# Kernel optimization log

Measured on AMD Instinct MI355X. Metric: run time of the kernel, lower is better.

The kernel has to match this reference:

```python
import jax, jax.numpy as jnp
import numpy as np
import math

N, CIN, COUT, K, H, W = 16, 512, 512, 1024, 64, 64


def setup_inputs() -> dict:
    key = jax.random.key(0)
    k0, k1, k2, k3, k4 = jax.random.split(key, 5)
    latent = jax.random.normal(k0, (N, CIN, H, W), dtype=jnp.float32)
    # kaiming_uniform_ on (K, COUT): bound = sqrt(6 / fan_in), fan_in = COUT
    cb_bound = math.sqrt(6.0 / COUT)
    codebook = jax.random.uniform(k1, (K, COUT), minval=-cb_bound, maxval=cb_bound, dtype=jnp.float32)
    # nn.Linear default init: uniform(-1/sqrt(fan_in), 1/sqrt(fan_in)), weight stored (out, in)
    wq = jax.random.uniform(k2, (COUT, CIN), minval=-1 / math.sqrt(CIN), maxval=1 / math.sqrt(CIN), dtype=jnp.float32)
    wk = jax.random.uniform(k3, (COUT, COUT), minval=-1 / math.sqrt(COUT), maxval=1 / math.sqrt(COUT), dtype=jnp.float32)
    wv = jax.random.uniform(k4, (COUT, COUT), minval=-1 / math.sqrt(COUT), maxval=1 / math.sqrt(COUT), dtype=jnp.float32)
    return {"latent": latent, "codebook": codebook, "wq": wq, "wk": wk, "wv": wv, "temperature": 1}


def _forward(latent, codebook, wq, wk, wv, temperature):
    n, cin, h, w = latent.shape
    kk, cout = codebook.shape
    scale = math.sqrt(cin)

    q = jnp.einsum("nchw,oc->nhwo", latent, wq)          # [n,h,w,cout]
    kmat = codebook @ wk.T                                   # [k,cout]
    v = codebook @ wv.T                                      # [k,cout]
    logit = jnp.einsum("nhwc,kc->nhwk", q, kmat) / scale  # [n,h,w,k]

    # ---- no-grad mask / histogram computation (dropout branch) ----
    lg = jax.lax.stop_gradient(logit)
    rk = jax.random.key(1234)
    r1, r2, r3 = jax.random.split(rk, 3)
    prob = jax.nn.softmax(lg, axis=-1)
    prob = jnp.where(prob < 1.0 / kk, 0.0, prob)
    mask = jax.random.bernoulli(r1, prob)                    # [n,h,w,k] bool
    trueCode = jnp.argmax(prob, axis=-1)                     # [n,h,w] int
    flat = trueCode.reshape(n, -1)
    binCount = jnp.zeros((n, kk), dtype=jnp.float32).at[jnp.arange(n)[:, None], flat].add(1.0)
    frequency = binCount[jnp.arange(n)[:, None, None], trueCode]  # [n,h,w]
    dropout = jax.random.bernoulli(r2, frequency / float(h * w))   # [n,h,w] bool
    scatterMask = jax.nn.one_hot(trueCode, kk, dtype=jnp.bool_) & dropout[..., None]
    mask = mask | scatterMask

    maskedLogit = jnp.where(mask, -1e9, logit)

    # ---- hard gumbel-softmax (straight-through) ----
    g = jax.random.gumbel(r3, maskedLogit.shape, dtype=maskedLogit.dtype)
    y_soft = jax.nn.softmax((maskedLogit + g) / temperature, axis=-1)
    y_hard = jax.nn.one_hot(jnp.argmax(y_soft, axis=-1), kk, dtype=y_soft.dtype)
    sample = y_hard - jax.lax.stop_gradient(y_soft) + y_soft

    result = jnp.einsum("nhwk,kc->nhwc", sample, v)
    quantized = jnp.transpose(result, (0, 3, 1, 2))          # [n,cout,h,w]
    code = jnp.argmax(sample, axis=-1)
    return quantized, code, logit, trueCode, frequency, binCount


def reference(latent, codebook, wq, wk, wv, temperature):
    return _forward(latent, codebook, wq, wk, wv, temperature)
```

## Files before the change

kernel.cpp:

```cpp
#include <hip/hip_runtime.h>
#include <stdint.h>
#include <stddef.h>

#define NB   16
#define CIN  512
#define COUT 512
#define KK   1024

#define MARGIN    2e-5f
#define INV_SCALE 0.04419417382415922f

typedef short short4v __attribute__((ext_vector_type(4)));
typedef short short8v __attribute__((ext_vector_type(8)));
typedef float f32x4  __attribute__((ext_vector_type(4)));

union Frag { short4v h[2]; short8v v8; };

__host__ __device__ inline void tf2x32(uint32_t k0, uint32_t k1,
                                       uint32_t x0, uint32_t x1,
                                       uint32_t& o0, uint32_t& o1) {
  uint32_t ks2 = k0 ^ k1 ^ 0x1BD11BDAu;
  x0 += k0; x1 += k1;
#define TF_RND(r) { x0 += x1; x1 = (x1 << r) | (x1 >> (32 - r)); x1 ^= x0; }
  TF_RND(13) TF_RND(15) TF_RND(26) TF_RND(6)
  x0 += k1;  x1 += ks2 + 1u;
  TF_RND(17) TF_RND(29) TF_RND(16) TF_RND(24)
  x0 += ks2; x1 += k0 + 2u;
  TF_RND(13) TF_RND(15) TF_RND(26) TF_RND(6)
  x0 += k0;  x1 += k1 + 3u;
  TF_RND(17) TF_RND(29) TF_RND(16) TF_RND(24)
  x0 += k1;  x1 += ks2 + 4u;
  TF_RND(13) TF_RND(15) TF_RND(26) TF_RND(6)
  x0 += ks2; x1 += k0 + 5u;
#undef TF_RND
  o0 = x0; o1 = x1;
}

__device__ inline float bits_to_u(uint32_t b) {
  return __uint_as_float((b >> 9) | 0x3f800000u) - 1.0f;
}

__device__ __host__ inline uint16_t f2bf(float f) {
  union { float f; uint32_t u; } c; c.f = f;
  uint32_t r = (c.u + 0x7fffu + ((c.u >> 16) & 1u)) >> 16;
  return (uint16_t)r;
}
__device__ inline float bf2f(uint16_t h) {
  union { uint32_t u; float f; } c; c.u = ((uint32_t)h) << 16;
  return c.f;
}

__device__ inline int permpos(int c) {
  const int base32 = c & ~31, within = c & 31;
  const int g = (within >> 2) & 3;
  const int e = (within & 16) ? (4 + (within & 3)) : (within & 3);
  return base32 + g * 8 + e;
}

__global__ __launch_bounds__(256) void k_combo(const float* __restrict__ cb,
                                               const float* __restrict__ wk,
                                               const float* __restrict__ wv,
                                               const float* __restrict__ latent,
                                               double* __restrict__ kmatT64,
                                               float* __restrict__ v,
                                               uint16_t* __restrict__ Apk) {
  __shared__ __align__(16) char sm[34816];
  const int t = threadIdx.x;
  if (blockIdx.x < 128) {
    float (*rows)[CIN] = (float(*)[CIN])sm;
    const int k0 = blockIdx.x * 8;
#pragma unroll
    for (int kk = 0; kk < 8; ++kk)
      for (int c = t; c < CIN; c += 256) rows[kk][c] = cb[(size_t)(k0 + kk) * CIN + c];
    __syncthreads();
#pragma unroll
    for (int oo = 0; oo < 2; ++oo) {
      const int o = t + oo * 256;
      const float* kr = wk + (size_t)o * CIN;
      const float* vr = wv + (size_t)o * CIN;
      double ak[8] = {0,0,0,0,0,0,0,0}, av[8] = {0,0,0,0,0,0,0,0};
      for (int c = 0; c < CIN; c += 4) {
        const float4 k4 = *(const float4*)(kr + c);
        const float4 v4 = *(const float4*)(vr + c);
#pragma unroll
        for (int kk = 0; kk < 8; ++kk) {
          const float4 c4 = *(const float4*)&rows[kk][c];
          ak[kk] += (double)c4.x * (double)k4.x + (double)c4.y * (double)k4.y
                  + (double)c4.z * (double)k4.z + (double)c4.w * (double)k4.w;
          av[kk] += (double)c4.x * (double)v4.x + (double)c4.y * (double)v4.y
                  + (double)c4.z * (double)v4.z + (double)c4.w * (double)v4.w;
        }
      }
#pragma unroll
      for (int kk = 0; kk < 8; ++kk) {
        kmatT64[(size_t)o * KK + k0 + kk] = ak[kk];
        v[(size_t)(k0 + kk) * COUT + o]  = (float)av[kk];
      }
    }
  } else {
    float (*T)[68] = (float(*)[68])sm;
    const int rb = blockIdx.x - 128, n = rb >> 6, h = rb & 63;
    for (int c0 = 0; c0 < 512; c0 += 128) {
      const int c2 = t >> 1, wh = (t & 1) * 32;
      const float* src = latent + (size_t)n * 2097152 + (size_t)(c0 + c2) * 4096 + h * 64 + wh;
#pragma unroll
      for (int i = 0; i < 8; ++i)
        *(float4*)&T[c2][wh + i*4] = *(const float4*)(src + i*4);
      __syncthreads();
      const int w = t & 63, cp = t >> 6;
      const int cs = (c0 >> 5) + cp;
      const int p = rb * 64 + w;
      uint16_t* dst = Apk + ((size_t)cs * 65536 + p) * 64;
#pragma unroll
      for (int q = 0; q < 8; ++q) {
        short8v vv;
#pragma unroll
        for (int j = 0; j < 4; ++j) {
          const float f = T[cp*32 + (q & 3) * 4 + (q >> 2) * 16 + j][w];
          const uint16_t hb = f2bf(f);
          vv[j]     = (short)hb;
          vv[4 + j] = (short)f2bf(f - bf2f(hb));
        }
        *(short8v*)(dst + q * 8) = vv;
      }
      __syncthreads();
    }
  }
}

__global__ __launch_bounds__(256) void k_wfold(const float* __restrict__ wq,
                                               const double* __restrict__ kmatT64,
                                               double* __restrict__ WT64,
                                               uint16_t* __restrict__ Wph,
                                               uint16_t* __restrict__ Wpl) {
  __shared__ __align__(16) float  As[16][64];
  __shared__ __align__(16) double Bs[16][128];
  const int t  = threadIdx.x;
  const int cb = (blockIdx.x >> 3) * 64;
  const int kb = (blockIdx.x & 7) * 128;
  const int tc = t >> 4, tk = t & 15;

  double acc[4][8];
#pragma unroll
  for (int i = 0; i < 4; ++i)
#pragma unroll
    for (int j = 0; j < 8; ++j) acc[i][j] = 0.0;

  for (int o0 = 0; o0 < COUT; o0 += 16) {
    {
      const int o2 = t >> 4, c4 = (t & 15) * 4;
      float4 f = *(const float4*)&wq[(size_t)(o0 + o2) * CIN + cb + c4];
      As[o2][c4+0] = f.x; As[o2][c4+1] = f.y; As[o2][c4+2] = f.z; As[o2][c4+3] = f.w;
    }
    {
      const int o2 = t >> 4, k8 = (t & 15) * 8;
      const double* src = &kmatT64[(size_t)(o0 + o2) * KK + kb + k8];
#pragma unroll
      for (int j = 0; j < 8; ++j) Bs[o2][k8 + j] = src[j];
    }
    __syncthreads();
#pragma unroll 4
    for (int o2 = 0; o2 < 16; ++o2) {
      double a[4], b[8];
#pragma unroll
      for (int i = 0; i < 4; ++i) a[i] = (double)As[o2][tc*4 + i];
#pragma unroll
      for (int j = 0; j < 8; ++j) b[j] = Bs[o2][tk*8 + j];
#pragma unroll
      for (int i = 0; i < 4; ++i)
#pragma unroll
        for (int j = 0; j < 8; ++j) acc[i][j] += a[i] * b[j];
    }
    __syncthreads();
  }
#pragma unroll
  for (int i = 0; i < 4; ++i) {
    const int c = cb + tc*4 + i;
    const int pp = permpos(c);
#pragma unroll
    for (int j = 0; j < 8; ++j) {
      const int k = kb + tk*8 + j;
      const double a = acc[i][j];
      WT64[(size_t)k * CIN + c] = a;
      const float wf = (float)a;
      const uint16_t hb = f2bf(wf);
      const float lof = wf - bf2f(hb);
      Wph[(size_t)k * CIN + pp] = hb;
      Wpl[(size_t)k * CIN + pp] = f2bf(lof);
    }
  }
}

#define STAGE_B(buf_, st_) do {                                            \
  const int kc_ = (st_) >> 4, cs_ = (st_) & 15;                            \
  _Pragma("unroll")                                                        \
  for (int i_ = 0; i_ < 8; ++i_) {                                         \
    const int half_ = i_ >> 2;                                             \
    const int D_ = (i_ & 3) * 4096 + wave * 1024 + lane * 16;              \
    const int kcol_ = D_ >> 6;                                             \
    const int bs_ = ((D_ >> 4) & 3) ^ ((kcol_ >> 1) & 3);                  \
    const uint16_t* gsrc_ = (half_ ? Wpl : Wph) +                          \
        ((size_t)(kc_ * 256 + kcol_) * 512 + cs_ * 32 + bs_ * 8);          \
    uint16_t* ldst_ = &Bst[buf_][half_ * 8192 + (D_ >> 1)];                \
    __builtin_amdgcn_global_load_lds(                                      \
        (const __attribute__((address_space(1))) uint32_t*)gsrc_,          \
        (__attribute__((address_space(3))) uint32_t*)ldst_, 16, 0, 0);     \
  } } while (0)

#define STAGE_A(buf_, st_) do {                                            \
  const int cs_ = (st_) & 15;                                              \
  _Pragma("unroll")                                                        \
  for (int i_ = 0; i_ < 2; ++i_) {                                         \
    const int D_ = i_ * 4096 + t * 16;                                     \
    const int row_ = D_ >> 7;                                              \
    const int q_ = ((D_ >> 4) & 7) ^ (row_ & 7);                           \
    const uint16_t* gsrc_ = Apk +                                          \
        ((size_t)cs_ * 65536 + pbase + row_) * 64 + q_ * 8;                \
    uint16_t* ldst_ = &Ast[buf_][D_ >> 1];                                 \
    __builtin_amdgcn_global_load_lds(                                      \
        (const __attribute__((address_space(1))) uint32_t*)gsrc_,          \
        (__attribute__((address_space(3))) uint32_t*)ldst_, 16, 0, 0);     \
  } } while (0)

__global__ __launch_bounds__(256, 2) void k_logit(
    const uint16_t* __restrict__ Apk,
    const uint16_t* __restrict__ Wph, const uint16_t* __restrict__ Wpl,
    const float* __restrict__ latent, const double* __restrict__ WT64,
    float* __restrict__ out_logit, int* __restrict__ trueCode, int* __restrict__ binCnt) {
  __shared__ __align__(16) char smem[81920];
  uint16_t (*Bst)[16384] = (uint16_t(*)[16384])smem;
  uint16_t (*Ast)[4096]  = (uint16_t(*)[4096])(smem + 65536);
  float* rv1     = (float*)(smem + 65536);
  int*   rk1     = (int*)  (smem + 65536 + 256);
  float* rv2     = (float*)(smem + 65536 + 512);
  int*   rk2     = (int*)  (smem + 65536 + 768);
  int*   candCnt = (int*)  (smem + 65536 + 1024);
  int  (*candK)[8] = (int(*)[8])(smem + 65536 + 1280);

  const int t = threadIdx.x;
  const int wave = t >> 6, lane = t & 63;
  const int wr = wave >> 1, wc = wave & 1;
  const int rb = blockIdx.x, n = rb >> 6;
  const int pbase = rb * 64;
  const int lg = lane >> 4, l15 = lane & 15;

  float v1_[2][4], v2_[2][4]; int k1_[2][4], k2_[2][4];
#pragma unroll
  for (int rt = 0; rt < 2; ++rt)
#pragma unroll
    for (int reg = 0; reg < 4; ++reg) {
      v1_[rt][reg] = -3.0e38f; k1_[rt][reg] = 0x7fffffff;
      v2_[rt][reg] = -3.0e38f; k2_[rt][reg] = 0x7fffffff;
    }

  f32x4 acc[2][8];

  STAGE_A(0, 0);
  STAGE_B(0, 0);
  __syncthreads();

  for (int st = 0; st < 64; ++st) {
    const int cur = st & 1, kc = st >> 4, cs = st & 15;
    if (cs == 0) {
#pragma unroll
      for (int rt = 0; rt < 2; ++rt)
#pragma unroll
        for (int ct = 0; ct < 8; ++ct) acc[rt][ct] = (f32x4){0.f, 0.f, 0.f, 0.f};
    }
    if (st < 63) { STAGE_A(cur ^ 1, st + 1); STAGE_B(cur ^ 1, st + 1); }

    Frag ah[2], al[2];
#pragma unroll
    for (int rt = 0; rt < 2; ++rt) {
      const int row = wr * 32 + rt * 16 + l15;
      const uint16_t* ab = &Ast[cur][row * 64];
      const int s0 = (lg ^ (row & 7)) * 8;
      Frag f0, f1;
      f0.v8 = *(const short8v*)(ab + s0);
      f1.v8 = *(const short8v*)(ab + (s0 ^ 32));
      ah[rt].h[0] = f0.h[0]; ah[rt].h[1] = f1.h[0];
      al[rt].h[0] = f0.h[1]; al[rt].h[1] = f1.h[1];
    }

#pragma unroll
    for (int ct = 0; ct < 8; ++ct) {
      const int kcol = wc * 128 + ct * 16 + l15;
      const int sw = lg ^ ((kcol >> 1) & 3);
      Frag bh, bl;
      bh.v8 = *(const short8v*)&Bst[cur][kcol * 32 + sw * 8];
      bl.v8 = *(const short8v*)&Bst[cur][8192 + kcol * 32 + sw * 8];
#pragma unroll
      for (int rt = 0; rt < 2; ++rt) {
        acc[rt][ct] = __builtin_amdgcn_mfma_f32_16x16x32_bf16(ah[rt].v8, bh.v8, acc[rt][ct], 0, 0, 0);
        acc[rt][ct] = __builtin_amdgcn_mfma_f32_16x16x32_bf16(ah[rt].v8, bl.v8, acc[rt][ct], 0, 0, 0);
        acc[rt][ct] = __builtin_amdgcn_mfma_f32_16x16x32_bf16(al[rt].v8, bh.v8, acc[rt][ct], 0, 0, 0);
      }
    }
    if (cs == 15) {
#pragma unroll
      for (int rt = 0; rt < 2; ++rt) {
#pragma unroll
        for (int reg = 0; reg < 4; ++reg) {
          const int prow = pbase + wr * 32 + rt * 16 + 4 * lg + reg;
          float* dst = out_logit + (size_t)prow * KK + kc * 256 + wc * 128 + l15;
          float v1 = v1_[rt][reg], v2 = v2_[rt][reg];
          int   k1 = k1_[rt][reg], k2 = k2_[rt][reg];
#pragma unroll
          for (int ct = 0; ct < 8; ++ct) {
            const float vv = acc[rt][ct][reg] * INV_SCALE;
            dst[ct * 16] = vv;
            const int kk = kc * 256 + wc * 128 + ct * 16 + l15;
            if (vv > v1 || (vv == v1 && kk < k1)) { v2 = v1; k2 = k1; v1 = vv; k1 = kk; }
            else if (vv > v2 || (vv == v2 && kk < k2)) { v2 = vv; k2 = kk; }
          }
          v1_[rt][reg] = v1; v2_[rt][reg] = v2;
          k1_[rt][reg] = k1; k2_[rt][reg] = k2;
        }
      }
    }
    __syncthreads();
  }

#pragma unroll
  for (int rt = 0; rt < 2; ++rt)
#pragma unroll
    for (int reg = 0; reg < 4; ++reg) {
      float v1 = v1_[rt][reg], v2 = v2_[rt][reg];
      int   k1 = k1_[rt][reg], k2 = k2_[rt][reg];
#pragma unroll
      for (int off = 1; off < 16; off <<= 1) {
        const float o1 = __shfl_xor(v1, off); const int ok1 = __shfl_xor(k1, off);
        const float o2 = __shfl_xor(v2, off); const int ok2 = __shfl_xor(k2, off);
        const bool aw = (v1 > o1) || (v1 == o1 && k1 < ok1);
        float n1, n2; int nk1, nk2;
        if (aw) {
          n1 = v1; nk1 = k1;
          if ((o1 > v2) || (o1 == v2 && ok1 < k2)) { n2 = o1; nk2 = ok1; }
          else { n2 = v2; nk2 = k2; }
        } else {
          n1 = o1; nk1 = ok1;
          if ((v1 > o2) || (v1 == o2 && k1 < ok2)) { n2 = v1; nk2 = k1; }
          else { n2 = o2; nk2 = ok2; }
        }
        v1 = n1; k1 = nk1; v2 = n2; k2 = nk2;
      }
      v1_[rt][reg] = v1; v2_[rt][reg] = v2;
      k1_[rt][reg] = k1; k2_[rt][reg] = k2;
    }
  if (wc == 0 && l15 == 0) {
#pragma unroll
    for (int rt = 0; rt < 2; ++rt)
#pragma unroll
      for (int reg = 0; reg < 4; ++reg) {
        const int r = wr * 32 + rt * 16 + 4 * lg + reg;
        rv1[r] = v1_[rt][reg]; rk1[r] = k1_[rt][reg];
        rv2[r] = v2_[rt][reg]; rk2[r] = k2_[rt][reg];
      }
  }
  __syncthreads();
  if (wc == 1 && l15 == 0) {
#pragma unroll
    for (int rt = 0; rt < 2; ++rt)
#pragma unroll
      for (int reg = 0; reg < 4; ++reg) {
        const int r = wr * 32 + rt * 16 + 4 * lg + reg;
        const float a1 = rv1[r], a2 = rv2[r];
        const int   ak1 = rk1[r], ak2 = rk2[r];
        const float b1 = v1_[rt][reg], b2 = v2_[rt][reg];
        const int   bk1 = k1_[rt][reg], bk2 = k2_[rt][reg];
        const bool aw = (a1 > b1) || (a1 == b1 && ak1 < bk1);
        float n1, n2; int nk1, nk2;
        if (aw) {
          n1 = a1; nk1 = ak1;
          if ((b1 > a2) || (b1 == a2 && bk1 < ak2)) { n2 = b1; nk2 = bk1; }
          else { n2 = a2; nk2 = ak2; }
        } else {
          n1 = b1; nk1 = bk1;
          if ((a1 > b2) || (a1 == b2 && ak1 < bk2)) { n2 = a1; nk2 = ak1; }
          else { n2 = b2; nk2 = bk2; }
        }
        rv1[r] = n1; rk1[r] = nk1; rv2[r] = n2; rk2[r] = nk2;
      }
  }
  __syncthreads();

  const int wv = t >> 6, lane_ = t & 63;
  for (int rr = 0; rr < 16; ++rr) {
    const int r = wv * 16 + rr;
    const int p = pbase + r;
    const float mv1 = rv1[r], mv2 = rv2[r];
    if (mv1 - mv2 > MARGIN) {
      if (lane_ == 0) {
        const int tc0 = rk1[r];
        trueCode[p] = tc0;
        atomicAdd(&binCnt[n * KK + tc0], 1);
      }
    } else {
      if (lane_ == 0) candCnt[r] = 0;
      __builtin_amdgcn_sched_barrier(0);
      asm volatile("s_waitcnt lgkmcnt(0)" ::: "memory");
      __builtin_amdgcn_sched_barrier(0);
      {
        const float thr = mv1 - MARGIN;
        const float* src = out_logit + (size_t)p * KK + lane_ * 16;
#pragma unroll
        for (int i = 0; i < 4; ++i) {
          const float4 f = *(const float4*)(src + i * 4);
          const int kb = lane_ * 16 + i * 4;
          if (f.x >= thr) { int id = atomicAdd(&candCnt[r], 1); if (id < 8) candK[r][id] = kb + 0; }
          if (f.y >= thr) { int id = atomicAdd(&candCnt[r], 1); if (id < 8) candK[r][id] = kb + 1; }
          if (f.z >= thr) { int id = atomicAdd(&candCnt[r], 1); if (id < 8) candK[r][id] = kb + 2; }
          if (f.w >= thr) { int id = atomicAdd(&candCnt[r], 1); if (id < 8) candK[r][id] = kb + 3; }
        }
      }
      __builtin_amdgcn_sched_barrier(0);
      asm volatile("s_waitcnt lgkmcnt(0)" ::: "memory");
      __builtin_amdgcn_sched_barrier(0);
      int cnt = candCnt[r]; if (cnt > 8) cnt = 8;
      const float* Ap = latent + (size_t)(p >> 12) * 2097152 + (p & 4095);
      int ks[8];
#pragma unroll
      for (int m = 0; m < 8; ++m) ks[m] = candK[r][m < cnt ? m : 0];
      double part[8] = {0, 0, 0, 0, 0, 0, 0, 0};
#pragma unroll
      for (int jj = 0; jj < 8; ++jj) {
        const int c = jj * 64 + lane_;
        const double lv = (double)Ap[(size_t)c * 4096];
#pragma unroll
        for (int m = 0; m < 8; ++m)
          if (m < cnt) part[m] += lv * WT64[(size_t)ks[m] * CIN + c];
      }
#pragma unroll
      for (int m = 0; m < 8; ++m)
        for (int off = 32; off; off >>= 1) part[m] += __shfl_xor(part[m], off);
      if (lane_ == 0) {
        double bv = -1.0e300; int bkk = KK;
#pragma unroll
        for (int m = 0; m < 8; ++m)
          if (m < cnt && (part[m] > bv || (part[m] == bv && ks[m] < bkk))) { bv = part[m]; bkk = ks[m]; }
        trueCode[p] = bkk;
        atomicAdd(&binCnt[n * KK + bkk], 1);
      }
    }
  }
}

__global__ __launch_bounds__(256) void k_final(const float* __restrict__ logit,
                                               const int* __restrict__ trueCode,
                                               const int* __restrict__ binCnt,
                                               float* __restrict__ out_code,
                                               float* __restrict__ out_tc,
                                               float* __restrict__ out_freq,
                                               int* __restrict__ code_int,
                                               uint32_t r1a, uint32_t r1b,
                                               uint32_t r2a, uint32_t r2b,
                                               uint32_t r3a, uint32_t r3b) {
  const int lane = threadIdx.x & 63;
  const int p = blockIdx.x * 4 + (threadIdx.x >> 6);
  const float* Lr = logit + (size_t)p * KK + lane * 16;

  float l[16];
#pragma unroll
  for (int i = 0; i < 4; ++i) {
    const float4 f = *(const float4*)(Lr + i * 4);
    l[i*4+0] = f.x; l[i*4+1] = f.y; l[i*4+2] = f.z; l[i*4+3] = f.w;
  }

  float m = l[0];
#pragma unroll
  for (int i = 1; i < 16; ++i) m = fmaxf(m, l[i]);
  for (int off = 32; off; off >>= 1) m = fmaxf(m, __shfl_xor(m, off));

  float e[16], s = 0.f;
#pragma unroll
  for (int i = 0; i < 16; ++i) { e[i] = __expf(l[i] - m); s += e[i]; }
  for (int off = 32; off; off >>= 1) s += __shfl_xor(s, off);

  const int tc = trueCode[p];
  const float fq = (float)binCnt[(p >> 12) * KK + tc];
  uint32_t d0, d1; tf2x32(r2a, r2b, 0u, (uint32_t)p, d0, d1);
  const bool drop = bits_to_u(d0 ^ d1) < fq * (1.0f / 4096.0f);

  const float thr = s * 0.0009765625f;
  float bv = -3.0e38f; int bk = 0;
#pragma unroll
  for (int j = 0; j < 16; ++j) {
    const int k = lane * 16 + j;
    const uint32_t idx = (uint32_t)(p * KK + k);
    uint32_t m0, m1, g0, g1;
    tf2x32(r1a, r1b, 0u, idx, m0, m1);
    tf2x32(r3a, r3b, 0u, idx, g0, g1);
    const bool mk = ((e[j] >= thr) && (bits_to_u(m0 ^ m1) * s < e[j])) || (k == tc && drop);
    const float u3  = fmaxf(bits_to_u(g0 ^ g1), 1.17549435082228751e-38f);
    const float gum = -__logf(-logf(u3));
    const float z = mk ? (gum - 1.0e9f) : (l[j] + gum);
    if (z > bv) { bv = z; bk = k; }
  }
  for (int off = 32; off; off >>= 1) {
    const float ov = __shfl_xor(bv, off);
    const int   ok = __shfl_xor(bk, off);
    if (ov > bv || (ov == bv && ok < bk)) { bv = ov; bk = ok; }
  }
  if (lane == 0) {
    out_code[p] = (float)bk; code_int[p] = bk;
    out_tc[p] = (float)tc;   out_freq[p] = fq;
  }
}

__global__ __launch_bounds__(256) void k_quant(const float* __restrict__ v,
                                               const int* __restrict__ code_int,
                                               float* __restrict__ outq) {
  __shared__ int codes[4096];
  const int n  = blockIdx.x >> 6;
  const int og = blockIdx.x & 63;
  const int t = threadIdx.x;
  const int4* cp = (const int4*)(code_int + (size_t)n * 4096);
#pragma unroll
  for (int i = 0; i < 4; ++i) ((int4*)codes)[t + i * 256] = cp[t + i * 256];
  __syncthreads();
  float* ob = outq + ((size_t)n * 512 + og * 8) * 4096;
  for (int c = 0; c < 4; ++c) {
    const int pos4 = (c * 256 + t) * 4;
    const int c0 = codes[pos4], c1 = codes[pos4 + 1], c2 = codes[pos4 + 2], c3 = codes[pos4 + 3];
    const float* v0 = v + (size_t)c0 * COUT;
    const float* v1 = v + (size_t)c1 * COUT;
    const float* v2 = v + (size_t)c2 * COUT;
    const float* v3 = v + (size_t)c3 * COUT;
#pragma unroll
    for (int oo = 0; oo < 8; ++oo) {
      const int o = og * 8 + oo;
      float4 val = make_float4(v0[o], v1[o], v2[o], v3[o]);
      *(float4*)(ob + (size_t)oo * 4096 + pos4) = val;
    }
  }
}

__global__ __launch_bounds__(256) void k_bincopy(const int* __restrict__ binCnt,
                                                 float* __restrict__ outb) {
  const int i = blockIdx.x * 256 + threadIdx.x;
  if (i < NB * KK) outb[i] = (float)binCnt[i];
}

extern "C" void kernel_launch(void* const* d_in, const int* in_sizes, int n_in,
                              void* d_out, int out_size, void* d_ws, size_t ws_size,
                              hipStream_t stream) {
  const float* latent   = (const float*)d_in[0];
  const float* codebook = (const float*)d_in[1];
  const float* wq       = (const float*)d_in[2];
  const float* wk       = (const float*)d_in[3];
  const float* wv       = (const float*)d_in[4];

  float* out = (float*)d_out;
  float* out_quant = out;
  float* out_code  = out + 33554432;
  float* out_logit = out + 33619968;
  float* out_tc    = out + 100728832;
  float* out_freq  = out + 100794368;
  float* out_bin   = out + 100859904;

  double*   WT64    = (double*)  out_quant;
  uint16_t* Wph     = (uint16_t*)(out_quant + 1048576);
  uint16_t* Wpl     = (uint16_t*)(out_quant + 1310720);
  double*   kmatT64 = (double*)  (out_quant + 1572864);

  char* ws = (char*)d_ws;
  uint16_t* Apk     = (uint16_t*)(ws);
  float*    v       = (float*)(ws + 134217728);
  int*      trueCode= (int*)  (ws + 136314880);
  int*      code_int= (int*)  (ws + 136577024);
  int*      binCnt  = (int*)  (ws + 136839168);

  uint32_t r1a, r1b, r2a, r2b, r3a, r3b;
  tf2x32(0u, 1234u, 0u, 0u, r1a, r1b);
  tf2x32(0u, 1234u, 0u, 1u, r2a, r2b);
  tf2x32(0u, 1234u, 0u, 2u, r3a, r3b);

  hipMemsetAsync(binCnt, 0, NB * KK * sizeof(int), stream);
  k_combo <<<1152,  256, 0, stream>>>(codebook, wk, wv, latent, kmatT64, v, Apk);
  k_wfold <<<64,    256, 0, stream>>>(wq, kmatT64, WT64, Wph, Wpl);
  k_logit <<<1024,  256, 0, stream>>>(Apk, Wph, Wpl, latent, WT64,
                                      out_logit, trueCode, binCnt);
  k_final <<<16384, 256, 0, stream>>>(out_logit, trueCode, binCnt,
                                      out_code, out_tc, out_freq, code_int,
                                      r1a, r1b, r2a, r2b, r3a, r3b);
  k_quant <<<1024,  256, 0, stream>>>(v, code_int, out_quant);
  k_bincopy<<<64,   256, 0, stream>>>(binCnt, out_bin);
}
```

Baseline: 909.2 us.

## Fuse gumbel sampling into logit kernel via two-candidate argmax, defer dropout pick

Moves the softmax/mask/gumbel argmax from the separate k_final kernel into the tail of k_logit. Because the dropout decision depends on global bin counts that are not known until k_logit finishes, each row keeps a top-two candidate: the code without dropout and the code if the true code were masked. A tiny k_pick kernel then chooses between them after the histogram is complete. The logit rows are re-read right after being written, so they are likely still in cache, and a full kernel launch over the logits is removed. The cost is extra register pressure and more work in the tail of k_logit, plus slightly more complex tie-breaking logic.

```diff
diff --git a/kernel.cpp b/kernel.cpp
--- a/kernel.cpp
+++ b/kernel.cpp
@@ -226,7 +226,9 @@
     const uint16_t* __restrict__ Apk,
     const uint16_t* __restrict__ Wph, const uint16_t* __restrict__ Wpl,
     const float* __restrict__ latent, const double* __restrict__ WT64,
-    float* __restrict__ out_logit, int* __restrict__ trueCode, int* __restrict__ binCnt) {
+    float* __restrict__ out_logit, int* __restrict__ trueCode, int* __restrict__ binCnt,
+    int* __restrict__ candA, int* __restrict__ candB,
+    uint32_t r1a, uint32_t r1b, uint32_t r3a, uint32_t r3b) {
   __shared__ __align__(16) char smem[81920];
   uint16_t (*Bst)[16384] = (uint16_t(*)[16384])smem;
   uint16_t (*Ast)[4096]  = (uint16_t(*)[4096])(smem + 65536);
@@ -440,71 +442,93 @@
           if (m < cnt && (part[m] > bv || (part[m] == bv && ks[m] < bkk))) { bv = part[m]; bkk = ks[m]; }
         trueCode[p] = bkk;
         atomicAdd(&binCnt[n * KK + bkk], 1);
-      }
-    }
-  }
-}
-
-__global__ __launch_bounds__(256) void k_final(const float* __restrict__ logit,
-                                               const int* __restrict__ trueCode,
-                                               const int* __restrict__ binCnt,
-                                               float* __restrict__ out_code,
-                                               float* __restrict__ out_tc,
-                                               float* __restrict__ out_freq,
-                                               int* __restrict__ code_int,
-                                               uint32_t r1a, uint32_t r1b,
-                                               uint32_t r2a, uint32_t r2b,
-                                               uint32_t r3a, uint32_t r3b) {
-  const int lane = threadIdx.x & 63;
-  const int p = blockIdx.x * 4 + (threadIdx.x >> 6);
-  const float* Lr = logit + (size_t)p * KK + lane * 16;
-
-  float l[16];
-#pragma unroll
-  for (int i = 0; i < 4; ++i) {
-    const float4 f = *(const float4*)(Lr + i * 4);
-    l[i*4+0] = f.x; l[i*4+1] = f.y; l[i*4+2] = f.z; l[i*4+3] = f.w;
-  }
-
-  float m = l[0];
-#pragma unroll
-  for (int i = 1; i < 16; ++i) m = fmaxf(m, l[i]);
-  for (int off = 32; off; off >>= 1) m = fmaxf(m, __shfl_xor(m, off));
-
-  float e[16], s = 0.f;
-#pragma unroll
-  for (int i = 0; i < 16; ++i) { e[i] = __expf(l[i] - m); s += e[i]; }
-  for (int off = 32; off; off >>= 1) s += __shfl_xor(s, off);
-
+        rk1[r] = bkk;
+      }
+    }
+  }
+  __syncthreads();
+
+  for (int rr = 0; rr < 16; ++rr) {
+    const int r = wv * 16 + rr;
+    const int p = pbase + r;
+    const float m = rv1[r];
+    const int  tc = rk1[r];
+    const float* Lr = out_logit + (size_t)p * KK + lane_ * 16;
+
+    float l[16];
+#pragma unroll
+    for (int i = 0; i < 4; ++i) {
+      const float4 f = *(const float4*)(Lr + i * 4);
+      l[i*4+0] = f.x; l[i*4+1] = f.y; l[i*4+2] = f.z; l[i*4+3] = f.w;
+    }
+    float e[16], s = 0.f;
+#pragma unroll
+    for (int i = 0; i < 16; ++i) { e[i] = __expf(l[i] - m); s += e[i]; }
+    for (int off = 32; off; off >>= 1) s += __shfl_xor(s, off);
+
+    const float thr = s * 0.0009765625f;
+    float z1 = -3.0e38f, z2 = -3.0e38f; int zk1 = 0x7fffffff, zk2 = 0x7fffffff;
+    float ztc = -3.0e38f;
+#pragma unroll
+    for (int j = 0; j < 16; ++j) {
+      const int k = lane_ * 16 + j;
+      const uint32_t idx = (uint32_t)(p * KK + k);
+      uint32_t m0, m1, g0, g1;
+      tf2x32(r1a, r1b, 0u, idx, m0, m1);
+      tf2x32(r3a, r3b, 0u, idx, g0, g1);
+      const bool bern = (e[j] >= thr) && (bits_to_u(m0 ^ m1) * s < e[j]);
+      const float u3  = fmaxf(bits_to_u(g0 ^ g1), 1.17549435082228751e-38f);
+      const float gum = -__logf(-logf(u3));
+      const float zmask = gum - 1.0e9f;
+      const float z = bern ? zmask : (l[j] + gum);
+      if (k == tc) ztc = zmask;
+      if (z > z1 || (z == z1 && k < zk1)) { z2 = z1; zk2 = zk1; z1 = z; zk1 = k; }
+      else if (z > z2 || (z == z2 && k < zk2)) { z2 = z; zk2 = k; }
+    }
+    for (int off = 1; off < 64; off <<= 1) {
+      const float o1 = __shfl_xor(z1, off); const int ok1 = __shfl_xor(zk1, off);
+      const float o2 = __shfl_xor(z2, off); const int ok2 = __shfl_xor(zk2, off);
+      const bool aw = (z1 > o1) || (z1 == o1 && zk1 < ok1);
+      float n1, n2; int nk1, nk2;
+      if (aw) {
+        n1 = z1; nk1 = zk1;
+        if ((o1 > z2) || (o1 == z2 && ok1 < zk2)) { n2 = o1; nk2 = ok1; }
+        else { n2 = z2; nk2 = zk2; }
+      } else {
+        n1 = o1; nk1 = ok1;
+        if ((z1 > o2) || (z1 == o2 && zk1 < ok2)) { n2 = z1; nk2 = zk1; }
+        else { n2 = o2; nk2 = ok2; }
+      }
+      z1 = n1; zk1 = nk1; z2 = n2; zk2 = nk2;
+      ztc = fmaxf(ztc, __shfl_xor(ztc, off));
+    }
+    if (lane_ == 0) {
+      candA[p] = zk1;
+      int cb_;
+      if (zk1 != tc) cb_ = zk1;
+      else cb_ = (z2 > ztc || (z2 == ztc && zk2 < tc)) ? zk2 : tc;
+      candB[p] = cb_;
+    }
+  }
+}
+
+__global__ __launch_bounds__(256) void k_pick(const int* __restrict__ trueCode,
+                                              const int* __restrict__ binCnt,
+                                              const int* __restrict__ candA,
+                                              const int* __restrict__ candB,
+                                              float* __restrict__ out_code,
+                                              float* __restrict__ out_tc,
+                                              float* __restrict__ out_freq,
+                                              int* __restrict__ code_int,
+                                              uint32_t r2a, uint32_t r2b) {
+  const int p = blockIdx.x * 256 + threadIdx.x;
   const int tc = trueCode[p];
   const float fq = (float)binCnt[(p >> 12) * KK + tc];
   uint32_t d0, d1; tf2x32(r2a, r2b, 0u, (uint32_t)p, d0, d1);
   const bool drop = bits_to_u(d0 ^ d1) < fq * (1.0f / 4096.0f);
-
-  const float thr = s * 0.0009765625f;
-  float bv = -3.0e38f; int bk = 0;
-#pragma unroll
-  for (int j = 0; j < 16; ++j) {
-    const int k = lane * 16 + j;
-    const uint32_t idx = (uint32_t)(p * KK + k);
-    uint32_t m0, m1, g0, g1;
-    tf2x32(r1a, r1b, 0u, idx, m0, m1);
-    tf2x32(r3a, r3b, 0u, idx, g0, g1);
-    const bool mk = ((e[j] >= thr) && (bits_to_u(m0 ^ m1) * s < e[j])) || (k == tc && drop);
-    const float u3  = fmaxf(bits_to_u(g0 ^ g1), 1.17549435082228751e-38f);
-    const float gum = -__logf(-logf(u3));
-    const float z = mk ? (gum - 1.0e9f) : (l[j] + gum);
-    if (z > bv) { bv = z; bk = k; }
-  }
-  for (int off = 32; off; off >>= 1) {
-    const float ov = __shfl_xor(bv, off);
-    const int   ok = __shfl_xor(bk, off);
-    if (ov > bv || (ov == bv && ok < bk)) { bv = ov; bk = ok; }
-  }
-  if (lane == 0) {
-    out_code[p] = (float)bk; code_int[p] = bk;
-    out_tc[p] = (float)tc;   out_freq[p] = fq;
-  }
+  const int code = drop ? candB[p] : candA[p];
+  out_code[p] = (float)code; code_int[p] = code;
+  out_tc[p] = (float)tc;     out_freq[p] = fq;
 }
 
 __global__ __launch_bounds__(256) void k_quant(const float* __restrict__ v,
@@ -569,6 +593,8 @@
   int*      trueCode= (int*)  (ws + 136314880);
   int*      code_int= (int*)  (ws + 136577024);
   int*      binCnt  = (int*)  (ws + 136839168);
+  int*      candA   = (int*)  (ws + 136904704);
+  int*      candB   = (int*)  (ws + 137166848);
 
   uint32_t r1a, r1b, r2a, r2b, r3a, r3b;
   tf2x32(0u, 1234u, 0u, 0u, r1a, r1b);
@@ -579,10 +605,10 @@
   k_combo <<<1152,  256, 0, stream>>>(codebook, wk, wv, latent, kmatT64, v, Apk);
   k_wfold <<<64,    256, 0, stream>>>(wq, kmatT64, WT64, Wph, Wpl);
   k_logit <<<1024,  256, 0, stream>>>(Apk, Wph, Wpl, latent, WT64,
-                                      out_logit, trueCode, binCnt);
-  k_final <<<16384, 256, 0, stream>>>(out_logit, trueCode, binCnt,
-                                      out_code, out_tc, out_freq, code_int,
-                                      r1a, r1b, r2a, r2b, r3a, r3b);
+                                      out_logit, trueCode, binCnt, candA, candB,
+                                      r1a, r1b, r3a, r3b);
+  k_pick  <<<256,   256, 0, stream>>>(trueCode, binCnt, candA, candB,
+                                      out_code, out_tc, out_freq, code_int, r2a, r2b);
   k_quant <<<1024,  256, 0, stream>>>(v, code_int, out_quant);
   k_bincopy<<<64,   256, 0, stream>>>(binCnt, out_bin);
 }
```

Result: slower. 959.7 us (+5.5%).
